# Optimization experiments

Measured on AMD Instinct MI355X. Metric: run time of the kernel, lower is better.

The kernel has to match this reference:

```python
import jax, jax.numpy as jnp
import numpy as np

N, FIN, FOUT = 4096, 256, 256


def setup_inputs() -> dict:
    key = jax.random.key(0)
    ks = jax.random.split(key, 6)
    x = jax.random.normal(ks[0], (N, FIN), jnp.float32)
    adj = jax.random.randint(ks[1], (N, N), 0, 2, jnp.int32)  # dense 0/1 adjacency
    W = jax.random.normal(ks[2], (FOUT, FIN), jnp.float32) / np.sqrt(FIN)
    b = jax.random.normal(ks[3], (FOUT,), jnp.float32) * 0.01
    att_w = jax.random.normal(ks[4], (2 * FOUT,), jnp.float32) / np.sqrt(2.0 * FOUT)  # Linear(2F,1).weight squeezed
    att_b = jax.random.normal(ks[5], (), jnp.float32) * 0.01
    return {"x": x, "adj": adj, "W": W, "b": b, "att_w": att_w, "att_b": att_b}


def reference(x, adj, W, b, att_w, att_b):
    n = x.shape[0]
    fo = W.shape[0]
    h = x @ W.T + b  # [N, Fout]
    # score(i,j) = att([h_i ; h_j]) = h_i.w1 + h_j.w2 + att_b  -> no [N,N,2F] concat
    s = (h @ att_w[:fo])[:, None] + (h @ att_w[fo:])[None, :] + att_b  # [N, N]
    edge = adj == 1
    # GLOBAL softmax over all edges (faithful to F.softmax(stacked_scores, dim=0))
    gmax = jnp.max(jnp.where(edge, s, -jnp.inf))
    e = jnp.exp(s - gmax)
    denom = jnp.sum(jnp.where(edge, e, 0.0))
    p = (e / denom).reshape(-1)  # softmaxed score per pair (valid at edges)
    # original indexes attention_scores[j] by NODE id j into the row-major edge list:
    # recover the score of the j-th global edge (j = 0..N-1) via cumsum rank + scatter
    flat = edge.reshape(-1)
    rank = jnp.cumsum(flat.astype(jnp.int32)) - 1  # rank of each edge in row-major order
    idx = jnp.where(flat, rank, n)  # non-edges and ranks >= n get dropped
    w_node = jnp.zeros((n,), h.dtype).at[idx].set(p, mode="drop")  # [N]
    # output[i] = sum_{j: adj[i,j]==1} w_node[j] * h[j]
    out = jax.nn.relu(edge.astype(h.dtype) @ (w_node[:, None] * h))
    return out
```

## Files before the change

### kernel.cpp

```cpp
#include <hip/hip_runtime.h>
#include <cstdint>
#include <cstddef>

#define NN 4096
#define FDIM 256

typedef __attribute__((ext_vector_type(4))) float fx4;
typedef __attribute__((ext_vector_type(2))) float fx2;
typedef __attribute__((ext_vector_type(8))) short s8v;

__device__ inline uint16_t f2bf(float f) {
    union { float f; uint32_t u; } v; v.f = f;
    uint32_t u = v.u;
    uint32_t r = (u + 0x7FFFu + ((u >> 16) & 1u)) >> 16;
    return (uint16_t)r;
}

__global__ __launch_bounds__(256) void k_h(const float* __restrict__ x,
        const float* __restrict__ W, const float* __restrict__ bias,
        const float* __restrict__ att_w, float* __restrict__ h,
        float* __restrict__ a1p, float* __restrict__ a2p) {
    __shared__ __align__(16) float xs[2][64 * 34];
    __shared__ __align__(16) float wt[2][64 * 68];
    const int bi = blockIdx.x, bf = blockIdx.y;
    const int t = threadIdx.x;
    const int tx = t & 15, ty = t >> 4;
    float acc[2][4] = {};
    float rx[8], rw[16];
    #pragma unroll
    for (int u = 0; u < 8; ++u) {
        const int e = t + 256 * u, r = e >> 6, c = e & 63;
        rx[u] = x[(size_t)(bi * 32 + r) * 256 + c];
    }
    #pragma unroll
    for (int u = 0; u < 16; ++u) {
        const int e = t + 256 * u, r = e >> 6, c = e & 63;
        rw[u] = W[(size_t)(bf * 64 + r) * 256 + c];
    }
    for (int p = 0; p < 4; ++p) {
        float* xb = xs[p & 1];
        float* wb = wt[p & 1];
        #pragma unroll
        for (int u = 0; u < 8; ++u) {
            const int e = t + 256 * u, r = e >> 6, c = e & 63;
            xb[c * 34 + r] = rx[u];
        }
        #pragma unroll
        for (int u = 0; u < 16; ++u) {
            const int e = t + 256 * u, r = e >> 6, c = e & 63;
            const int sw = 8 * ((c & 7) ^ ((c >> 3) & 7));
            wb[c * 68 + (r ^ sw)] = rw[u];
        }
        __syncthreads();
        if (p < 3) {
            const int k0 = (p + 1) * 64;
            #pragma unroll
            for (int u = 0; u < 8; ++u) {
                const int e = t + 256 * u, r = e >> 6, c = e & 63;
                rx[u] = x[(size_t)(bi * 32 + r) * 256 + k0 + c];
            }
            #pragma unroll
            for (int u = 0; u < 16; ++u) {
                const int e = t + 256 * u, r = e >> 6, c = e & 63;
                rw[u] = W[(size_t)(bf * 64 + r) * 256 + k0 + c];
            }
        }
        #pragma unroll 16
        for (int k = 0; k < 64; ++k) {
            const int sw = 8 * ((k & 7) ^ ((k >> 3) & 7));
            const fx2 av = *(const fx2*)(xb + k * 34 + ty * 2);
            const fx4 bv = *(const fx4*)(wb + k * 68 + ((tx * 4) ^ sw));
            #pragma unroll
            for (int u = 0; u < 2; ++u)
                #pragma unroll
                for (int v = 0; v < 4; ++v)
                    acc[u][v] += av[u] * bv[v];
        }
    }
    const fx4 bv = *(const fx4*)(bias + bf * 64 + tx * 4);
    const fx4 w1v = *(const fx4*)(att_w + bf * 64 + tx * 4);
    const fx4 w2v = *(const fx4*)(att_w + 256 + bf * 64 + tx * 4);
    #pragma unroll
    for (int u = 0; u < 2; ++u) {
        const int i = bi * 32 + ty * 2 + u;
        fx4 r;
        float s1 = 0.f, s2 = 0.f;
        #pragma unroll
        for (int v = 0; v < 4; ++v) {
            r[v] = acc[u][v] + bv[v];
            s1 += r[v] * w1v[v];
            s2 += r[v] * w2v[v];
        }
        *(fx4*)(h + (size_t)i * 256 + bf * 64 + tx * 4) = r;
        #pragma unroll
        for (int d = 8; d > 0; d >>= 1) {
            s1 += __shfl_down(s1, d, 16);
            s2 += __shfl_down(s2, d, 16);
        }
        if (tx == 0) {
            a1p[bf * NN + i] = s1;
            a2p[bf * NN + i] = s2;
        }
    }
}

__global__ __launch_bounds__(1024) void k_prep(const float* __restrict__ a1p,
        const float* __restrict__ a2p, const int* __restrict__ adj,
        float* __restrict__ E1, float* __restrict__ E2,
        float* __restrict__ wraw, float* __restrict__ Sg) {
    __shared__ float E1s[NN];
    __shared__ float E2s[NN];
    __shared__ float red1[16], red2[16];
    __shared__ int wtot[16];
    __shared__ int base_s;
    const int t = threadIdx.x, lane = t & 63, wv = t >> 6;
    fx4 v1 = {0.f, 0.f, 0.f, 0.f}, v2 = {0.f, 0.f, 0.f, 0.f};
    #pragma unroll
    for (int bf = 0; bf < 4; ++bf) {
        v1 += *(const fx4*)(a1p + bf * NN + t * 4);
        v2 += *(const fx4*)(a2p + bf * NN + t * 4);
    }
    float m1 = fmaxf(fmaxf(v1[0], v1[1]), fmaxf(v1[2], v1[3]));
    float m2 = fmaxf(fmaxf(v2[0], v2[1]), fmaxf(v2[2], v2[3]));
    #pragma unroll
    for (int d = 32; d > 0; d >>= 1) {
        m1 = fmaxf(m1, __shfl_down(m1, d));
        m2 = fmaxf(m2, __shfl_down(m2, d));
    }
    if (lane == 0) { red1[wv] = m1; red2[wv] = m2; }
    __syncthreads();
    if (t == 0) {
        float mm1 = -1e30f, mm2 = -1e30f;
        for (int k = 0; k < 16; ++k) {
            mm1 = fmaxf(mm1, red1[k]);
            mm2 = fmaxf(mm2, red2[k]);
        }
        red1[0] = mm1; red2[0] = mm2;
        *Sg = 0.f;
        base_s = 0;
    }
    __syncthreads();
    const float M1 = red1[0], M2 = red2[0];
    fx4 e1v, e2v, z4 = {0.f, 0.f, 0.f, 0.f};
    #pragma unroll
    for (int j = 0; j < 4; ++j) {
        e1v[j] = expf(v1[j] - M1);
        e2v[j] = expf(v2[j] - M2);
    }
    *(fx4*)(E1s + t * 4) = e1v;
    *(fx4*)(E2s + t * 4) = e2v;
    *(fx4*)(E1 + t * 4) = e1v;
    *(fx4*)(E2 + t * 4) = e2v;
    *(fx4*)(wraw + t * 4) = z4;
    __syncthreads();
    for (int row = 0; row < NN; ++row) {
        const int base = base_s;
        if (base >= NN) break;
        const int4 a = ((const int4*)(adj + (size_t)row * NN))[t];
        const int vj[4] = {a.x, a.y, a.z, a.w};
        int cnt = 0;
        #pragma unroll
        for (int j = 0; j < 4; ++j) cnt += (vj[j] == 1);
        int inc = cnt;
        #pragma unroll
        for (int d = 1; d < 64; d <<= 1) {
            const int y = __shfl_up(inc, d);
            if (lane >= d) inc += y;
        }
        if (lane == 63) wtot[wv] = inc;
        __syncthreads();
        int wbase = 0, total = 0;
        #pragma unroll
        for (int w = 0; w < 16; ++w) {
            const int xw = wtot[w];
            total += xw;
            wbase += (w < wv) ? xw : 0;
        }
        if (t == 0) base_s = base + total;
        int r = base + wbase + inc - cnt;
        if (cnt && r < NN) {
            const float e1 = E1s[row];
            #pragma unroll
            for (int j = 0; j < 4; ++j) {
                if (vj[j] == 1) {
                    if (r < NN) wraw[r] = e1 * E2s[t * 4 + j];
                    ++r;
                }
            }
        }
        __syncthreads();
    }
}

__global__ __launch_bounds__(256) void k_g(const float* __restrict__ h,
        const float* __restrict__ wraw, uint16_t* __restrict__ gt) {
    __shared__ float tile[32 * 65];
    const int bj = blockIdx.x, bf = blockIdx.y;
    const int j0 = bj * 32, f0 = bf * 64;
    const int t = threadIdx.x;
    #pragma unroll
    for (int p = 0; p < 8; ++p) {
        const int e = t + 256 * p;
        const int jl = e >> 6, fl = e & 63;
        tile[jl * 65 + fl] = h[(size_t)(j0 + jl) * 256 + f0 + fl] * wraw[j0 + jl];
    }
    __syncthreads();
    #pragma unroll
    for (int p = 0; p < 8; ++p) {
        const int e = t + 256 * p;
        const int fl = e >> 5, jl = e & 31;
        gt[(size_t)(f0 + fl) * NN + j0 + jl] = f2bf(tile[jl * 65 + fl]);
    }
}

__global__ __launch_bounds__(256) void k_fused(const int* __restrict__ adj,
        const uint16_t* __restrict__ gt, const float* __restrict__ E1,
        const float* __restrict__ E2, uint16_t* __restrict__ part,
        float* __restrict__ Sg, int krange) {
    __shared__ __align__(16) uint16_t As[64 * 72];
    __shared__ __align__(16) uint16_t Gs[272 * 72];
    const int ib = blockIdx.x, ks = blockIdx.y;
    const int t = threadIdx.x;
    const int wv = t >> 6, lane = t & 63;
    const int q = lane >> 4, m16 = lane & 15;
    const int i0 = ib * 64, k0 = ks * krange;
    const int ksteps = krange >> 6;
    fx4 acc[4][4];
    #pragma unroll
    for (int a = 0; a < 4; ++a)
        #pragma unroll
        for (int b = 0; b < 4; ++b) acc[a][b] = (fx4){0.f, 0.f, 0.f, 0.f};
    fx4 accS[4];
    #pragma unroll
    for (int a = 0; a < 4; ++a) accS[a] = (fx4){0.f, 0.f, 0.f, 0.f};
    for (int e = t; e < 15 * 72; e += 256) Gs[257 * 72 + e] = 0;
    for (int step = 0; step < ksteps; ++step) {
        const int kk = k0 + step * 64;
        #pragma unroll
        for (int p = 0; p < 4; ++p) {
            const int r = p * 16 + (t >> 4);
            const int c4 = (t & 15) * 4;
            const int4 a = *(const int4*)(adj + (size_t)(i0 + r) * NN + kk + c4);
            uint2 w;
            w.x = (uint32_t)(a.x | (a.y << 16)) * 0x3F80u;
            w.y = (uint32_t)(a.z | (a.w << 16)) * 0x3F80u;
            *(uint2*)(&As[r * 72 + c4]) = w;
        }
        #pragma unroll
        for (int p = 0; p < 8; ++p) {
            const int f = p * 32 + (t >> 3);
            const int ch = (t & 7) * 8;
            const s8v v = *(const s8v*)(gt + (size_t)f * NN + kk + ch);
            *(s8v*)(Gs + f * 72 + ch) = v;
        }
        if (t < 8) {
            const float* e2p = E2 + kk + t * 8;
            uint32_t* dst = (uint32_t*)(&Gs[256 * 72 + t * 8]);
            #pragma unroll
            for (int j = 0; j < 4; ++j)
                dst[j] = (uint32_t)f2bf(e2p[2 * j]) |
                         ((uint32_t)f2bf(e2p[2 * j + 1]) << 16);
        }
        __syncthreads();
        s8v afr[4][2];
        #pragma unroll
        for (int it = 0; it < 4; ++it)
            #pragma unroll
            for (int kh = 0; kh < 2; ++kh)
                afr[it][kh] = *(const s8v*)(As + (it * 16 + m16) * 72 + kh * 32 + q * 8);
        #pragma unroll
        for (int ft = 0; ft < 4; ++ft) {
            #pragma unroll
            for (int kh = 0; kh < 2; ++kh) {
                const s8v bfr = *(const s8v*)(Gs + (wv * 64 + ft * 16 + m16) * 72 + kh * 32 + q * 8);
                #pragma unroll
                for (int it = 0; it < 4; ++it)
                    acc[it][ft] = __builtin_amdgcn_mfma_f32_16x16x32_bf16(
                        afr[it][kh], bfr, acc[it][ft], 0, 0, 0);
            }
        }
        if (wv == 3) {
            #pragma unroll
            for (int kh = 0; kh < 2; ++kh) {
                const s8v bfrS = *(const s8v*)(Gs + (256 + m16) * 72 + kh * 32 + q * 8);
                #pragma unroll
                for (int it = 0; it < 4; ++it)
                    accS[it] = __builtin_amdgcn_mfma_f32_16x16x32_bf16(
                        afr[it][kh], bfrS, accS[it], 0, 0, 0);
            }
        }
        __syncthreads();
    }
    if (wv == 3) {
        float s_local = 0.f;
        #pragma unroll
        for (int it = 0; it < 4; ++it)
            #pragma unroll
            for (int r = 0; r < 4; ++r)
                s_local += accS[it][r] * E1[i0 + it * 16 + q * 4 + r];
        #pragma unroll
        for (int d = 32; d > 0; d >>= 1) s_local += __shfl_down(s_local, d);
        if (lane == 0) atomicAdd(Sg, s_local);
    }
    uint16_t* dst = part + (size_t)ks * NN * FDIM;
    #pragma unroll
    for (int it = 0; it < 4; ++it) {
        #pragma unroll
        for (int ft = 0; ft < 4; ++ft) {
            const int f = wv * 64 + ft * 16 + m16;
            #pragma unroll
            for (int r = 0; r < 4; ++r) {
                const int i = i0 + it * 16 + q * 4 + r;
                dst[(size_t)i * FDIM + f] = f2bf(acc[it][ft][r]);
            }
        }
    }
}

__global__ __launch_bounds__(256) void k_out(const uint16_t* __restrict__ part,
        const float* __restrict__ Sg, float* __restrict__ out, int nsplit) {
    const size_t idx = ((size_t)blockIdx.x * 256 + threadIdx.x) * 8;
    const float inv = 1.0f / (*Sg);
    float s[8] = {};
    for (int k = 0; k < nsplit; ++k) {
        const s8v v = *(const s8v*)(part + (size_t)k * NN * FDIM + idx);
        #pragma unroll
        for (int j = 0; j < 8; ++j) {
            union { uint32_t u; float f; } cv;
            cv.u = ((uint32_t)(uint16_t)v[j]) << 16;
            s[j] += cv.f;
        }
    }
    fx4 r0, r1;
    #pragma unroll
    for (int j = 0; j < 4; ++j) {
        r0[j] = fmaxf(s[j], 0.f) * inv;
        r1[j] = fmaxf(s[4 + j], 0.f) * inv;
    }
    *(fx4*)(out + idx) = r0;
    *(fx4*)(out + idx + 4) = r1;
}

extern "C" void kernel_launch(void* const* d_in, const int* in_sizes, int n_in,
                              void* d_out, int out_size, void* d_ws, size_t ws_size,
                              hipStream_t stream) {
    const float* x     = (const float*)d_in[0];
    const int*   adj   = (const int*)d_in[1];
    const float* W     = (const float*)d_in[2];
    const float* bias  = (const float*)d_in[3];
    const float* att_w = (const float*)d_in[4];
    float* out = (float*)d_out;
    char* ws = (char*)d_ws;
    float*    h    = (float*)(ws + 0);
    uint16_t* gt   = (uint16_t*)(ws + (size_t)4194304);
    float*    a1p  = (float*)(ws + 6291456);
    float*    a2p  = (float*)(ws + 6356992);
    float*    E1   = (float*)(ws + 6422528);
    float*    E2   = (float*)(ws + 6438912);
    float*    wraw = (float*)(ws + 6455296);
    float*    Sg   = (float*)(ws + 6471680);
    uint16_t* part = (uint16_t*)(ws + 6471936);

    const size_t avail = (ws_size > 6471936) ? (ws_size - 6471936) : 0;
    int splitk = 1;
    while (splitk < 8 &&
           (size_t)(splitk * 2) * NN * FDIM * sizeof(uint16_t) <= avail)
        splitk <<= 1;
    const int krange = NN / splitk;

    k_h    <<<dim3(128, 4), 256, 0, stream>>>(x, W, bias, att_w, h, a1p, a2p);
    k_prep <<<dim3(1), 1024, 0, stream>>>(a1p, a2p, adj, E1, E2, wraw, Sg);
    k_g    <<<dim3(128, 4), 256, 0, stream>>>(h, wraw, gt);
    k_fused<<<dim3(64, splitk), 256, 0, stream>>>(adj, gt, E1, E2, part, Sg, krange);
    k_out  <<<dim3(512), 256, 0, stream>>>(part, Sg, out, splitk);
}
```

Measured before the change: 152.3 us.

## Load G tiles via global_load_lds with XOR swizzle; enlarge k_h/k_g tiles

```diff
diff --git a/kernel.cpp b/kernel.cpp
--- a/kernel.cpp
+++ b/kernel.cpp
@@ -20,58 +20,45 @@
         const float* __restrict__ W, const float* __restrict__ bias,
         const float* __restrict__ att_w, float* __restrict__ h,
         float* __restrict__ a1p, float* __restrict__ a2p) {
-    __shared__ __align__(16) float xs[2][64 * 34];
-    __shared__ __align__(16) float wt[2][64 * 68];
+    __shared__ __align__(16) float xs[64 * 68];
+    __shared__ __align__(16) float wt[64 * 68];
     const int bi = blockIdx.x, bf = blockIdx.y;
     const int t = threadIdx.x;
     const int tx = t & 15, ty = t >> 4;
-    float acc[2][4] = {};
-    float rx[8], rw[16];
-    #pragma unroll
-    for (int u = 0; u < 8; ++u) {
-        const int e = t + 256 * u, r = e >> 6, c = e & 63;
-        rx[u] = x[(size_t)(bi * 32 + r) * 256 + c];
-    }
+    float acc[4][4] = {};
+    float rx[16], rw[16];
     #pragma unroll
     for (int u = 0; u < 16; ++u) {
         const int e = t + 256 * u, r = e >> 6, c = e & 63;
+        rx[u] = x[(size_t)(bi * 64 + r) * 256 + c];
         rw[u] = W[(size_t)(bf * 64 + r) * 256 + c];
     }
     for (int p = 0; p < 4; ++p) {
-        float* xb = xs[p & 1];
-        float* wb = wt[p & 1];
-        #pragma unroll
-        for (int u = 0; u < 8; ++u) {
-            const int e = t + 256 * u, r = e >> 6, c = e & 63;
-            xb[c * 34 + r] = rx[u];
-        }
+        if (p) __syncthreads();
         #pragma unroll
         for (int u = 0; u < 16; ++u) {
             const int e = t + 256 * u, r = e >> 6, c = e & 63;
             const int sw = 8 * ((c & 7) ^ ((c >> 3) & 7));
-            wb[c * 68 + (r ^ sw)] = rw[u];
+            xs[c * 68 + (r ^ sw)] = rx[u];
+            wt[c * 68 + (r ^ sw)] = rw[u];
         }
         __syncthreads();
         if (p < 3) {
             const int k0 = (p + 1) * 64;
             #pragma unroll
-            for (int u = 0; u < 8; ++u) {
-                const int e = t + 256 * u, r = e >> 6, c = e & 63;
-                rx[u] = x[(size_t)(bi * 32 + r) * 256 + k0 + c];
-            }
-            #pragma unroll
             for (int u = 0; u < 16; ++u) {
                 const int e = t + 256 * u, r = e >> 6, c = e & 63;
+                rx[u] = x[(size_t)(bi * 64 + r) * 256 + k0 + c];
                 rw[u] = W[(size_t)(bf * 64 + r) * 256 + k0 + c];
             }
         }
-        #pragma unroll 16
+        #pragma unroll 8
         for (int k = 0; k < 64; ++k) {
             const int sw = 8 * ((k & 7) ^ ((k >> 3) & 7));
-            const fx2 av = *(const fx2*)(xb + k * 34 + ty * 2);
-            const fx4 bv = *(const fx4*)(wb + k * 68 + ((tx * 4) ^ sw));
-            #pragma unroll
-            for (int u = 0; u < 2; ++u)
+            const fx4 av = *(const fx4*)(xs + k * 68 + ((ty * 4) ^ sw));
+            const fx4 bv = *(const fx4*)(wt + k * 68 + ((tx * 4) ^ sw));
+            #pragma unroll
+            for (int u = 0; u < 4; ++u)
                 #pragma unroll
                 for (int v = 0; v < 4; ++v)
                     acc[u][v] += av[u] * bv[v];
@@ -81,8 +68,8 @@
     const fx4 w1v = *(const fx4*)(att_w + bf * 64 + tx * 4);
     const fx4 w2v = *(const fx4*)(att_w + 256 + bf * 64 + tx * 4);
     #pragma unroll
-    for (int u = 0; u < 2; ++u) {
-        const int i = bi * 32 + ty * 2 + u;
+    for (int u = 0; u < 4; ++u) {
+        const int i = bi * 64 + ty * 4 + u;
         fx4 r;
         float s1 = 0.f, s2 = 0.f;
         #pragma unroll
@@ -194,22 +181,27 @@
 
 __global__ __launch_bounds__(256) void k_g(const float* __restrict__ h,
         const float* __restrict__ wraw, uint16_t* __restrict__ gt) {
-    __shared__ float tile[32 * 65];
+    __shared__ float tile[64 * 65];
     const int bj = blockIdx.x, bf = blockIdx.y;
-    const int j0 = bj * 32, f0 = bf * 64;
+    const int j0 = bj * 64, f0 = bf * 64;
     const int t = threadIdx.x;
     #pragma unroll
-    for (int p = 0; p < 8; ++p) {
+    for (int p = 0; p < 16; ++p) {
         const int e = t + 256 * p;
         const int jl = e >> 6, fl = e & 63;
         tile[jl * 65 + fl] = h[(size_t)(j0 + jl) * 256 + f0 + fl] * wraw[j0 + jl];
     }
     __syncthreads();
     #pragma unroll
-    for (int p = 0; p < 8; ++p) {
-        const int e = t + 256 * p;
-        const int fl = e >> 5, jl = e & 31;
-        gt[(size_t)(f0 + fl) * NN + j0 + jl] = f2bf(tile[jl * 65 + fl]);
+    for (int u = 0; u < 2; ++u) {
+        const int unit = t + 256 * u;
+        const int fl = unit >> 3, cb = unit & 7;
+        const int phys_cb = cb ^ (fl & 7);
+        s8v v;
+        #pragma unroll
+        for (int lo = 0; lo < 8; ++lo)
+            v[lo] = (short)f2bf(tile[(cb * 8 + lo) * 65 + fl]);
+        *(s8v*)(gt + (size_t)(f0 + fl) * NN + j0 + phys_cb * 8) = v;
     }
 }
 
@@ -218,7 +210,8 @@
         const float* __restrict__ E2, uint16_t* __restrict__ part,
         float* __restrict__ Sg, int krange) {
     __shared__ __align__(16) uint16_t As[64 * 72];
-    __shared__ __align__(16) uint16_t Gs[272 * 72];
+    __shared__ __align__(16) uint16_t Gs[256 * 64];
+    __shared__ __align__(16) uint16_t GsS[16 * 72];
     const int ib = blockIdx.x, ks = blockIdx.y;
     const int t = threadIdx.x;
     const int wv = t >> 6, lane = t & 63;
@@ -233,7 +226,9 @@
     fx4 accS[4];
     #pragma unroll
     for (int a = 0; a < 4; ++a) accS[a] = (fx4){0.f, 0.f, 0.f, 0.f};
-    for (int e = t; e < 15 * 72; e += 256) Gs[257 * 72 + e] = 0;
+    for (int e = t; e < 15 * 72; e += 256) GsS[72 + e] = 0;
+
+    const int fr = lane >> 3, cb = lane & 7;
     for (int step = 0; step < ksteps; ++step) {
         const int kk = k0 + step * 64;
         #pragma unroll
@@ -248,14 +243,16 @@
         }
         #pragma unroll
         for (int p = 0; p < 8; ++p) {
-            const int f = p * 32 + (t >> 3);
-            const int ch = (t & 7) * 8;
-            const s8v v = *(const s8v*)(gt + (size_t)f * NN + kk + ch);
-            *(s8v*)(Gs + f * 72 + ch) = v;
+            const int f0 = wv * 64 + p * 8;
+            const uint16_t* gp = gt + (size_t)(f0 + fr) * NN + kk + cb * 8;
+            __builtin_amdgcn_global_load_lds(
+                (const __attribute__((address_space(1))) uint32_t*)gp,
+                (__attribute__((address_space(3))) uint32_t*)(Gs + f0 * 64),
+                16, 0, 0);
         }
         if (t < 8) {
             const float* e2p = E2 + kk + t * 8;
-            uint32_t* dst = (uint32_t*)(&Gs[256 * 72 + t * 8]);
+            uint32_t* dst = (uint32_t*)(&GsS[t * 8]);
             #pragma unroll
             for (int j = 0; j < 4; ++j)
                 dst[j] = (uint32_t)f2bf(e2p[2 * j]) |
@@ -272,7 +269,9 @@
         for (int ft = 0; ft < 4; ++ft) {
             #pragma unroll
             for (int kh = 0; kh < 2; ++kh) {
-                const s8v bfr = *(const s8v*)(Gs + (wv * 64 + ft * 16 + m16) * 72 + kh * 32 + q * 8);
+                const int row = wv * 64 + ft * 16 + m16;
+                const int pcb = ((kh << 2) | q) ^ (m16 & 7);
+                const s8v bfr = *(const s8v*)(Gs + row * 64 + pcb * 8);
                 #pragma unroll
                 for (int it = 0; it < 4; ++it)
                     acc[it][ft] = __builtin_amdgcn_mfma_f32_16x16x32_bf16(
@@ -282,7 +281,7 @@
         if (wv == 3) {
             #pragma unroll
             for (int kh = 0; kh < 2; ++kh) {
-                const s8v bfrS = *(const s8v*)(Gs + (256 + m16) * 72 + kh * 32 + q * 8);
+                const s8v bfrS = *(const s8v*)(GsS + m16 * 72 + kh * 32 + q * 8);
                 #pragma unroll
                 for (int it = 0; it < 4; ++it)
                     accS[it] = __builtin_amdgcn_mfma_f32_16x16x32_bf16(
@@ -368,9 +367,9 @@
         splitk <<= 1;
     const int krange = NN / splitk;
 
-    k_h    <<<dim3(128, 4), 256, 0, stream>>>(x, W, bias, att_w, h, a1p, a2p);
+    k_h    <<<dim3(64, 4), 256, 0, stream>>>(x, W, bias, att_w, h, a1p, a2p);
     k_prep <<<dim3(1), 1024, 0, stream>>>(a1p, a2p, adj, E1, E2, wraw, Sg);
-    k_g    <<<dim3(128, 4), 256, 0, stream>>>(h, wraw, gt);
+    k_g    <<<dim3(64, 4), 256, 0, stream>>>(h, wraw, gt);
     k_fused<<<dim3(64, splitk), 256, 0, stream>>>(adj, gt, E1, E2, part, Sg, krange);
     k_out  <<<dim3(512), 256, 0, stream>>>(part, Sg, out, splitk);
 }
```

Result: slower. 159.2 us (+4.5%).

## Pre-swizzle gt layout and load G tiles directly into LDS

Applied to the files above, without the earlier changes.

```diff
diff --git a/kernel.cpp b/kernel.cpp
--- a/kernel.cpp
+++ b/kernel.cpp
@@ -194,22 +194,25 @@
 
 __global__ __launch_bounds__(256) void k_g(const float* __restrict__ h,
         const float* __restrict__ wraw, uint16_t* __restrict__ gt) {
-    __shared__ float tile[32 * 65];
+    __shared__ float tile[64 * 33];
     const int bj = blockIdx.x, bf = blockIdx.y;
-    const int j0 = bj * 32, f0 = bf * 64;
+    const int j0 = bj * 64, f0 = bf * 32;
     const int t = threadIdx.x;
     #pragma unroll
     for (int p = 0; p < 8; ++p) {
         const int e = t + 256 * p;
-        const int jl = e >> 6, fl = e & 63;
-        tile[jl * 65 + fl] = h[(size_t)(j0 + jl) * 256 + f0 + fl] * wraw[j0 + jl];
+        const int jl = e >> 5, fl = e & 31;
+        tile[jl * 33 + fl] = h[(size_t)(j0 + jl) * 256 + f0 + fl] * wraw[j0 + jl];
     }
     __syncthreads();
-    #pragma unroll
-    for (int p = 0; p < 8; ++p) {
-        const int e = t + 256 * p;
-        const int fl = e >> 5, jl = e & 31;
-        gt[(size_t)(f0 + fl) * NN + j0 + jl] = f2bf(tile[jl * 65 + fl]);
+    {
+        const int fl = t >> 3, cb = t & 7;
+        const int phys_cb = cb ^ (fl & 7);
+        s8v v;
+        #pragma unroll
+        for (int lo = 0; lo < 8; ++lo)
+            v[lo] = (short)f2bf(tile[(cb * 8 + lo) * 33 + fl]);
+        *(s8v*)(gt + (size_t)(f0 + fl) * NN + j0 + phys_cb * 8) = v;
     }
 }
 
@@ -218,7 +221,8 @@
         const float* __restrict__ E2, uint16_t* __restrict__ part,
         float* __restrict__ Sg, int krange) {
     __shared__ __align__(16) uint16_t As[64 * 72];
-    __shared__ __align__(16) uint16_t Gs[272 * 72];
+    __shared__ __align__(16) uint16_t Gs[256 * 64];
+    __shared__ __align__(16) uint16_t GsS[16 * 72];
     const int ib = blockIdx.x, ks = blockIdx.y;
     const int t = threadIdx.x;
     const int wv = t >> 6, lane = t & 63;
@@ -233,7 +237,9 @@
     fx4 accS[4];
     #pragma unroll
     for (int a = 0; a < 4; ++a) accS[a] = (fx4){0.f, 0.f, 0.f, 0.f};
-    for (int e = t; e < 15 * 72; e += 256) Gs[257 * 72 + e] = 0;
+    for (int e = t; e < 15 * 72; e += 256) GsS[72 + e] = 0;
+
+    const int fr = lane >> 3, cb = lane & 7;
     for (int step = 0; step < ksteps; ++step) {
         const int kk = k0 + step * 64;
         #pragma unroll
@@ -248,14 +254,16 @@
         }
         #pragma unroll
         for (int p = 0; p < 8; ++p) {
-            const int f = p * 32 + (t >> 3);
-            const int ch = (t & 7) * 8;
-            const s8v v = *(const s8v*)(gt + (size_t)f * NN + kk + ch);
-            *(s8v*)(Gs + f * 72 + ch) = v;
+            const int f0 = wv * 64 + p * 8;
+            const uint16_t* gp = gt + (size_t)(f0 + fr) * NN + kk + cb * 8;
+            __builtin_amdgcn_global_load_lds(
+                (const __attribute__((address_space(1))) uint32_t*)gp,
+                (__attribute__((address_space(3))) uint32_t*)(Gs + f0 * 64),
+                16, 0, 0);
         }
         if (t < 8) {
             const float* e2p = E2 + kk + t * 8;
-            uint32_t* dst = (uint32_t*)(&Gs[256 * 72 + t * 8]);
+            uint32_t* dst = (uint32_t*)(&GsS[t * 8]);
             #pragma unroll
             for (int j = 0; j < 4; ++j)
                 dst[j] = (uint32_t)f2bf(e2p[2 * j]) |
@@ -272,7 +280,9 @@
         for (int ft = 0; ft < 4; ++ft) {
             #pragma unroll
             for (int kh = 0; kh < 2; ++kh) {
-                const s8v bfr = *(const s8v*)(Gs + (wv * 64 + ft * 16 + m16) * 72 + kh * 32 + q * 8);
+                const int row = wv * 64 + ft * 16 + m16;
+                const int pcb = ((kh << 2) | q) ^ (m16 & 7);
+                const s8v bfr = *(const s8v*)(Gs + row * 64 + pcb * 8);
                 #pragma unroll
                 for (int it = 0; it < 4; ++it)
                     acc[it][ft] = __builtin_amdgcn_mfma_f32_16x16x32_bf16(
@@ -282,7 +292,7 @@
         if (wv == 3) {
             #pragma unroll
             for (int kh = 0; kh < 2; ++kh) {
-                const s8v bfrS = *(const s8v*)(Gs + (256 + m16) * 72 + kh * 32 + q * 8);
+                const s8v bfrS = *(const s8v*)(GsS + m16 * 72 + kh * 32 + q * 8);
                 #pragma unroll
                 for (int it = 0; it < 4; ++it)
                     accS[it] = __builtin_amdgcn_mfma_f32_16x16x32_bf16(
@@ -370,7 +380,7 @@
 
     k_h    <<<dim3(128, 4), 256, 0, stream>>>(x, W, bias, att_w, h, a1p, a2p);
     k_prep <<<dim3(1), 1024, 0, stream>>>(a1p, a2p, adj, E1, E2, wraw, Sg);
-    k_g    <<<dim3(128, 4), 256, 0, stream>>>(h, wraw, gt);
+    k_g    <<<dim3(64, 8), 256, 0, stream>>>(h, wraw, gt);
     k_fused<<<dim3(64, splitk), 256, 0, stream>>>(adj, gt, E1, E2, part, Sg, krange);
     k_out  <<<dim3(512), 256, 0, stream>>>(part, Sg, out, splitk);
 }
```

Result: no change. 151.1 us (-0.8%).
